# Kernel optimization log

Measured on AMD Instinct MI355X. Metric: run time of the kernel, lower is better.

Reference implementation:

```python
import jax, jax.numpy as jnp
import numpy as np

N, C, H, W = 8, 19, 512, 512
BORDER_DILATE = 5
BORDER_POWER = 0.5
BORDER_WEIGHT = 1.0
IGNORE = 255


def setup_inputs() -> dict:
    key = jax.random.key(0)
    k1, k2 = jax.random.split(key)
    slices = jax.random.normal(k1, (N, C, H, W), dtype=jnp.float32)
    targets = jax.random.randint(k2, (N, 1, H, W), 0, C).astype(jnp.int64)
    return {"slices": slices, "targets": targets}


def class_boundaries(m):
    # m: bool (N, K, H, W); XOR of vertical/horizontal neighbors, padded like torch
    tb = m[:, :, 1:, :] ^ m[:, :, :-1, :]          # pad bottom row with 0
    lr = m[:, :, :, 1:] ^ m[:, :, :, :-1]          # pad leftmost column with 0
    tb = jnp.pad(tb, ((0, 0), (0, 0), (0, 1), (0, 0)))
    lr = jnp.pad(lr, ((0, 0), (0, 0), (0, 0), (1, 0)))
    return tb | lr


def _min_scan_axis(d, axis):
    # forward then backward chamfer pass d[i] = min(d[i], d[i -/+ 1] + 1) along `axis`
    x = jnp.moveaxis(d, axis, 0)

    def step(carry, row):
        new = jnp.minimum(row, carry + 1.0)
        return new, new

    _, fwd = jax.lax.scan(step, x[0], x[1:])
    x = jnp.concatenate([x[:1], fwd], axis=0)
    _, bwd = jax.lax.scan(step, x[-1], x[:-1][::-1])
    x = jnp.concatenate([bwd[::-1], x[-1:]], axis=0)
    return jnp.moveaxis(x, 0, axis)


def distance_matrix(border):
    # border: bool (N, K, H, W). Penalty matches torch.tensor((N,1,H,W)).sum()
    penalty = jnp.float32(N + 1 + H + W)
    d = jnp.where(border, 0.0, penalty)
    d = _min_scan_axis(d, 2)   # H forward + backward
    d = _min_scan_axis(d, 3)   # W forward + backward
    return jax.nn.relu(d - jnp.float32(BORDER_DILATE))


def _forward(slices, targets):
    t = targets[:, 0]  # (N, H, W)
    # cross-entropy, reduction='sum', ignore_index
    logp = jax.nn.log_softmax(slices, axis=1)
    valid = t != IGNORE
    t_safe = jnp.where(valid, t, 0)
    picked = jnp.take_along_axis(logp, t_safe[:, None], axis=1)[:, 0]  # (N,H,W)
    ce = -jnp.sum(jnp.where(valid, picked, 0.0))

    # border loss: vectorized over all class ids (torch loops over unique targets)
    sm = jax.nn.softmax(slices, axis=1)                      # (N,C,H,W)
    pred = jnp.argmax(slices, axis=1, keepdims=True)         # (N,1,H,W)
    cls = jnp.arange(C)[None, :, None, None]
    pred_oh = pred == cls                                    # (N,C,H,W) bool
    tgt_oh = targets == cls                                  # (N,C,H,W) bool
    pred_b = class_boundaries(pred_oh).astype(sm.dtype)
    tgt_d = distance_matrix(class_boundaries(tgt_oh))
    present = jnp.any(tgt_oh, axis=(0, 2, 3)).astype(sm.dtype)  # only ids in targets
    border = jnp.sum(sm * pred_b * tgt_d * present[None, :, None, None])

    return ce + jnp.float32(BORDER_WEIGHT) * border ** jnp.float32(BORDER_POWER)


def reference(slices, targets):
    return _forward(slices, targets)
```

## Files before the change

### kernel.cpp

```cpp
#include <hip/hip_runtime.h>

#define NN 8
#define CC 19
#define HH 512
#define WW 512
#define HW (HH*WW)
#define NPIX (NN*HW)
#define NPLANE (NN*CC)
#define BIGV (1<<20)
#define M7 0x7F7F7F7Fu

__device__ unsigned char g_tT[NPIX];
__device__ unsigned char g_pred[NPIX];
__device__ float g_lse[NPIX];
__device__ unsigned char g_inter[(size_t)NPLANE*HW];
__device__ unsigned char g_pbb[(size_t)NPLANE*HW/8];
__device__ float g_ce;
__device__ float g_part[64][16];
__device__ unsigned int g_present_mask;

__device__ __forceinline__ unsigned int eqz(unsigned int x) {
  unsigned int y = (x & M7) + M7;
  return ~(y | x | M7);
}

__global__ __launch_bounds__(256) void k_pixel(const float* __restrict__ slices,
                                               const int* __restrict__ targets) {
  int bp = blockIdx.x * 2048;
  int n = bp >> 18;
  int r = bp & (HW - 1);
  int wv = threadIdx.x >> 6;
  int lane = threadIdx.x & 63;
  int o0 = wv * 512 + lane * 4;
  int o1 = o0 + 256;
  const float* base = slices + (size_t)n * CC * HW + r;

  const int4* t4p = (const int4*)(targets + bp);
  int4 ta = t4p[o0 >> 2];
  int4 tb = t4p[o1 >> 2];
  int t[8] = {ta.x, ta.y, ta.z, ta.w, tb.x, tb.y, tb.z, tb.w};

  float m[8], s[8], pk[8];
  int a[8];
  {
    float4 x0 = *(const float4*)(base + o0);
    float4 x1 = *(const float4*)(base + o1);
    float x[8] = {x0.x, x0.y, x0.z, x0.w, x1.x, x1.y, x1.z, x1.w};
#pragma unroll
    for (int j = 0; j < 8; ++j) {
      m[j] = x[j];
      a[j] = 0;
      s[j] = __expf(x[j]);
      pk[j] = (t[j] == 0) ? x[j] : 0.f;
    }
  }
#pragma unroll 2
  for (int c = 1; c < CC; ++c) {
    float4 x0 = *(const float4*)(base + (size_t)c * HW + o0);
    float4 x1 = *(const float4*)(base + (size_t)c * HW + o1);
    float x[8] = {x0.x, x0.y, x0.z, x0.w, x1.x, x1.y, x1.z, x1.w};
#pragma unroll
    for (int j = 0; j < 8; ++j) {
      if (x[j] > m[j]) { m[j] = x[j]; a[j] = c; }
      s[j] += __expf(x[j]);
      pk[j] = (c == t[j]) ? x[j] : pk[j];
    }
  }

  float l[8];
  float ce_local = 0.f;
  unsigned int msk = 0u;
#pragma unroll
  for (int j = 0; j < 8; ++j) {
    l[j] = __logf(s[j]);
    if (t[j] != 255) ce_local += l[j] - pk[j];
    if ((unsigned)t[j] < CC) msk |= 1u << t[j];
  }

  ((float4*)(g_lse + bp))[o0 >> 2] = make_float4(l[0], l[1], l[2], l[3]);
  ((float4*)(g_lse + bp))[o1 >> 2] = make_float4(l[4], l[5], l[6], l[7]);
  ((uchar4*)(g_pred + bp))[o0 >> 2] =
      make_uchar4((unsigned char)a[0], (unsigned char)a[1],
                  (unsigned char)a[2], (unsigned char)a[3]);
  ((uchar4*)(g_pred + bp))[o1 >> 2] =
      make_uchar4((unsigned char)a[4], (unsigned char)a[5],
                  (unsigned char)a[6], (unsigned char)a[7]);
#pragma unroll
  for (int j = 0; j < 8; ++j) {
    int p = bp + ((j < 4) ? (o0 + j) : (o1 + j - 4));
    int h = (p >> 9) & 511;
    int w = p & 511;
    g_tT[((size_t)n << 18) + (size_t)w * HH + h] = (unsigned char)t[j];
  }

  __shared__ float sred[256];
  __shared__ unsigned int smsk[256];
  sred[threadIdx.x] = ce_local;
  smsk[threadIdx.x] = msk;
  __syncthreads();
  for (int st = 128; st > 0; st >>= 1) {
    if (threadIdx.x < st) {
      sred[threadIdx.x] += sred[threadIdx.x + st];
      smsk[threadIdx.x] |= smsk[threadIdx.x + st];
    }
    __syncthreads();
  }
  if (threadIdx.x == 0) {
    atomicAdd(&g_ce, sred[0]);
    atomicOr(&g_present_mask, smsk[0]);
  }
}

__global__ __launch_bounds__(512) void k_pbb() {
  int plane = blockIdx.x >> 3;
  int wt = blockIdx.x & 7;
  int c = plane % CC;
  int n = plane / CC;
  int h = threadIdx.x;

  const unsigned char* row = g_pred + ((size_t)n * HH + h) * WW + wt * 64;
  const unsigned char* rown = (h + 1 < HH) ? row + WW : row;

  uint4 c0 = *(const uint4*)(row);
  uint4 c1 = *(const uint4*)(row + 16);
  uint4 c2 = *(const uint4*)(row + 32);
  uint4 c3 = *(const uint4*)(row + 48);
  uint4 n0 = *(const uint4*)(rown);
  uint4 n1 = *(const uint4*)(rown + 16);
  uint4 n2 = *(const uint4*)(rown + 32);
  uint4 n3 = *(const uint4*)(rown + 48);
  unsigned int cwv[16] = {c0.x,c0.y,c0.z,c0.w, c1.x,c1.y,c1.z,c1.w,
                          c2.x,c2.y,c2.z,c2.w, c3.x,c3.y,c3.z,c3.w};
  unsigned int nwv[16] = {n0.x,n0.y,n0.z,n0.w, n1.x,n1.y,n1.z,n1.w,
                          n2.x,n2.y,n2.z,n2.w, n3.x,n3.y,n3.z,n3.w};
  int leftb = (wt > 0) ? (int)row[-1] : (int)(cwv[0] & 255u);

  unsigned char outb[8];
  int pl = leftb;
#pragma unroll
  for (int j = 0; j < 8; ++j) {
    unsigned int bits = 0u;
#pragma unroll
    for (int k = 0; k < 8; ++k) {
      int q = j * 8 + k;
      int pc = (int)((cwv[q >> 2] >> ((q & 3) * 8)) & 255u);
      int pn = (int)((nwv[q >> 2] >> ((q & 3) * 8)) & 255u);
      bool ec = (pc == c);
      bool bb = (ec != (pn == c)) || (ec != (pl == c));
      bits |= (bb ? 1u : 0u) << k;
      pl = pc;
    }
    outb[j] = (unsigned char)bits;
  }
  unsigned char* dst = g_pbb + (((size_t)plane * 8 + wt) * HH + h) * 8;
  *(uint2*)dst = *(const uint2*)outb;
}

__global__ __launch_bounds__(512, 4) void k_hscan() {
  int plane = blockIdx.x >> 3;
  int wt = blockIdx.x & 7;
  int hc = threadIdx.x >> 6;
  int wl = threadIdx.x & 63;
  int c = plane % CC;
  int n = plane / CC;
  int w = wt * 64 + wl;
  const unsigned char* colC = g_tT + ((size_t)n << 18) + (size_t)w * HH + hc * 64;

  uint4 ca = *(const uint4*)(colC);
  uint4 cb = *(const uint4*)(colC + 16);
  uint4 cc2 = *(const uint4*)(colC + 32);
  uint4 cd = *(const uint4*)(colC + 48);
  unsigned int cw[16];
  cw[0]=ca.x; cw[1]=ca.y; cw[2]=ca.z; cw[3]=ca.w;
  cw[4]=cb.x; cw[5]=cb.y; cw[6]=cb.z; cw[7]=cb.w;
  cw[8]=cc2.x; cw[9]=cc2.y; cw[10]=cc2.z; cw[11]=cc2.w;
  cw[12]=cd.x; cw[13]=cd.y; cw[14]=cd.z; cw[15]=cd.w;

  unsigned int lw[16];
#pragma unroll
  for (int i = 0; i < 16; ++i) lw[i] = __shfl_up(cw[i], 1, 64);
  if (wl == 0) {
    if (w > 0) {
      const unsigned char* colL = colC - HH;
      uint4 la = *(const uint4*)(colL);
      uint4 lb = *(const uint4*)(colL + 16);
      uint4 lc = *(const uint4*)(colL + 32);
      uint4 ld = *(const uint4*)(colL + 48);
      lw[0]=la.x; lw[1]=la.y; lw[2]=la.z; lw[3]=la.w;
      lw[4]=lb.x; lw[5]=lb.y; lw[6]=lb.z; lw[7]=lb.w;
      lw[8]=lc.x; lw[9]=lc.y; lw[10]=lc.z; lw[11]=lc.w;
      lw[12]=ld.x; lw[13]=ld.y; lw[14]=ld.z; lw[15]=ld.w;
    } else {
#pragma unroll
      for (int i = 0; i < 16; ++i) lw[i] = cw[i];
    }
  }

  __shared__ unsigned char s_edge[8][64];
  s_edge[hc][wl] = (unsigned char)(cw[0] & 255u);
  __syncthreads();
  unsigned int tnl = (hc < 7) ? (unsigned int)s_edge[hc + 1][wl]
                              : ((cw[15] >> 24) & 255u);

  unsigned int bc = (unsigned int)c * 0x01010101u;
  int v[64];
  int prev = BIGV;
#pragma unroll
  for (int i = 0; i < 16; ++i) {
    unsigned int cwi = cw[i];
    unsigned int nxt = (i < 15) ? (cw[i + 1] & 255u) : tnl;
    unsigned int tnw = (cwi >> 8) | (nxt << 24);
    unsigned int zc = eqz(cwi ^ bc);
    unsigned int zn = eqz(tnw ^ bc);
    unsigned int zl = eqz(lw[i] ^ bc);
    unsigned int bb = (zc ^ zn) | (zc ^ zl);
#pragma unroll
    for (int k = 0; k < 4; ++k) {
      int bit = (int)((bb >> (8 * k + 7)) & 1u);
      prev = min(bit ? 0 : 255, prev + 1);
      v[4 * i + k] = prev;
    }
  }

  __shared__ int s_car[8][64];
  s_car[hc][wl] = v[63];
  __syncthreads();
  int F = BIGV;
#pragma unroll
  for (int i = 0; i < 7; ++i)
    if (i < hc) F = min(s_car[i][wl] + 1, F + 64);
#pragma unroll
  for (int k = 0; k < 64; ++k) v[k] = min(v[k], F + k);

#pragma unroll
  for (int k = 62; k >= 0; --k) v[k] = min(v[k], v[k + 1] + 1);

  __syncthreads();
  s_car[hc][wl] = v[0];
  __syncthreads();
  int B = BIGV;
#pragma unroll
  for (int j = 7; j >= 1; --j)
    if (j > hc) B = min(s_car[j][wl] + 1, B + 64);

  unsigned char* outb = g_inter + (((size_t)plane * 8 + wt) * HH + hc * 64) * 64 + wl;
#pragma unroll
  for (int k = 0; k < 64; ++k) {
    int outv = min(v[k], B + (63 - k));
    outb[(size_t)k * 64] = (unsigned char)outv;
  }
}

__global__ __launch_bounds__(512) void k_wscan(const float* __restrict__ slices) {
  int plane = blockIdx.x >> 6;
  int hg = blockIdx.x & 63;
  int wv = threadIdx.x >> 6;
  int lane = threadIdx.x & 63;
  int h = hg * 8 + wv;
  int c = plane % CC;
  int n = plane / CC;

  const unsigned char* rowp =
      g_inter + (((size_t)plane * 8 + (lane >> 3)) * HH + h) * 64 + (lane & 7) * 8;
  uint2 r8 = *(const uint2*)rowp;
  unsigned int pbb = (unsigned int)
      g_pbb[(((size_t)plane * 8 + (lane >> 3)) * HH + h) * 8 + (lane & 7)];

  int d0[8];
#pragma unroll
  for (int k = 0; k < 4; ++k) {
    d0[k]     = (int)((r8.x >> (k * 8)) & 255u);
    d0[k + 4] = (int)((r8.y >> (k * 8)) & 255u);
  }
  int ls[8];
  ls[0] = d0[0];
#pragma unroll
  for (int k = 1; k < 8; ++k) ls[k] = min(d0[k], ls[k - 1] + 1);
  int u = ls[7] - 8 * lane;
#pragma unroll
  for (int o = 1; o < 64; o <<= 1) {
    int t = __shfl_up(u, o, 64);
    if (lane >= o) u = min(u, t);
  }
  int cf = __shfl_up(u, 1, 64);
  int carry = (lane == 0) ? BIGV : cf + 8 * (lane - 1);
  int f[8];
#pragma unroll
  for (int k = 0; k < 8; ++k) f[k] = min(ls[k], carry + k + 1);
  int bs[8];
  bs[7] = f[7];
#pragma unroll
  for (int k = 6; k >= 0; --k) bs[k] = min(f[k], bs[k + 1] + 1);
  int mm = bs[0] + 8 * lane;
#pragma unroll
  for (int o = 1; o < 64; o <<= 1) {
    int t = __shfl_down(mm, o, 64);
    if (lane + o < 64) mm = min(mm, t);
  }
  int mb = __shfl_down(mm, 1, 64);
  int carryb = (lane == 63) ? BIGV : mb - 8 * lane;

  float acc = 0.f;
#pragma unroll
  for (int k = 0; k < 8; ++k) {
    int D = min(bs[k], carryb - k);
    int d = D - 5;
    if (d > 0 && ((pbb >> k) & 1u)) {
      int w = lane * 8 + k;
      int pix = (n * HH + h) * WW + w;
      float x = slices[((size_t)n * CC + c) * HW + (size_t)h * WW + w];
      float smv = __expf(x - g_lse[pix]);
      acc += smv * (float)d;
    }
  }

#pragma unroll
  for (int o = 32; o > 0; o >>= 1) acc += __shfl_down(acc, o, 64);
  if (lane == 0) {
    float pres = (g_present_mask >> c) & 1u ? 1.f : 0.f;
    atomicAdd(&g_part[blockIdx.x & 63][0], acc * pres);
  }
}

__global__ void k_final(float* __restrict__ out) {
  int t = threadIdx.x;
  float b = g_part[t][0];
#pragma unroll
  for (int o = 32; o > 0; o >>= 1) b += __shfl_down(b, o, 64);
  if (t == 0) {
    out[0] = g_ce + sqrtf(b);
    g_ce = 0.f;
    g_present_mask = 0u;
  }
  g_part[t][0] = 0.f;
}

extern "C" void kernel_launch(void* const* d_in, const int* in_sizes, int n_in,
                              void* d_out, int out_size, void* d_ws, size_t ws_size,
                              hipStream_t stream) {
  const float* slices = (const float*)d_in[0];
  const int* targets = (const int*)d_in[1];
  float* out = (float*)d_out;
  (void)d_ws; (void)ws_size; (void)in_sizes; (void)n_in; (void)out_size;

  hipLaunchKernelGGL(k_pixel, dim3(NPIX / 2048), dim3(256), 0, stream, slices, targets);
  hipLaunchKernelGGL(k_pbb, dim3(NPLANE * 8), dim3(512), 0, stream);
  hipLaunchKernelGGL(k_hscan, dim3(NPLANE * 8), dim3(512), 0, stream);
  hipLaunchKernelGGL(k_wscan, dim3(NPLANE * 64), dim3(512), 0, stream, slices);
  hipLaunchKernelGGL(k_final, dim3(1), dim3(64), 0, stream, out);
}
```

Before: 117.9 us.

## Fuse pred-border kernel into hscan, stage target tile in LDS, fold final reduction

Merges the predicted-boundary bitmask computation into the horizontal scan kernel, which removes one launch. The transposed target tile is now staged through shared memory with a padded stride, so each column and its left neighbour are read from LDS instead of coalescing-poor global loads and shuffles. The final reduction kernel is replaced by a last-block-done pattern using an atomic counter inside k_wscan, which saves another launch. The cost is a large 33KB LDS allocation in k_hscan, which may lower occupancy, plus extra fences and atomics at the end of every wscan block.

Measured after the change: 347.0 us. 194% more time.

```diff
diff --git a/kernel.cpp b/kernel.cpp
--- a/kernel.cpp
+++ b/kernel.cpp
@@ -18,6 +18,7 @@
 __device__ float g_ce;
 __device__ float g_part[64][16];
 __device__ unsigned int g_present_mask;
+__device__ unsigned int g_done;
 
 __device__ __forceinline__ unsigned int eqz(unsigned int x) {
   unsigned int y = (x & M7) + M7;
@@ -111,51 +112,7 @@
   }
 }
 
-__global__ __launch_bounds__(512) void k_pbb() {
-  int plane = blockIdx.x >> 3;
-  int wt = blockIdx.x & 7;
-  int c = plane % CC;
-  int n = plane / CC;
-  int h = threadIdx.x;
-
-  const unsigned char* row = g_pred + ((size_t)n * HH + h) * WW + wt * 64;
-  const unsigned char* rown = (h + 1 < HH) ? row + WW : row;
-
-  uint4 c0 = *(const uint4*)(row);
-  uint4 c1 = *(const uint4*)(row + 16);
-  uint4 c2 = *(const uint4*)(row + 32);
-  uint4 c3 = *(const uint4*)(row + 48);
-  uint4 n0 = *(const uint4*)(rown);
-  uint4 n1 = *(const uint4*)(rown + 16);
-  uint4 n2 = *(const uint4*)(rown + 32);
-  uint4 n3 = *(const uint4*)(rown + 48);
-  unsigned int cwv[16] = {c0.x,c0.y,c0.z,c0.w, c1.x,c1.y,c1.z,c1.w,
-                          c2.x,c2.y,c2.z,c2.w, c3.x,c3.y,c3.z,c3.w};
-  unsigned int nwv[16] = {n0.x,n0.y,n0.z,n0.w, n1.x,n1.y,n1.z,n1.w,
-                          n2.x,n2.y,n2.z,n2.w, n3.x,n3.y,n3.z,n3.w};
-  int leftb = (wt > 0) ? (int)row[-1] : (int)(cwv[0] & 255u);
-
-  unsigned char outb[8];
-  int pl = leftb;
-#pragma unroll
-  for (int j = 0; j < 8; ++j) {
-    unsigned int bits = 0u;
-#pragma unroll
-    for (int k = 0; k < 8; ++k) {
-      int q = j * 8 + k;
-      int pc = (int)((cwv[q >> 2] >> ((q & 3) * 8)) & 255u);
-      int pn = (int)((nwv[q >> 2] >> ((q & 3) * 8)) & 255u);
-      bool ec = (pc == c);
-      bool bb = (ec != (pn == c)) || (ec != (pl == c));
-      bits |= (bb ? 1u : 0u) << k;
-      pl = pc;
-    }
-    outb[j] = (unsigned char)bits;
-  }
-  unsigned char* dst = g_pbb + (((size_t)plane * 8 + wt) * HH + h) * 8;
-  *(uint2*)dst = *(const uint2*)outb;
-}
-
+#define CSTRIDE 528
 __global__ __launch_bounds__(512, 4) void k_hscan() {
   int plane = blockIdx.x >> 3;
   int wt = blockIdx.x & 7;
@@ -164,42 +121,85 @@
   int c = plane % CC;
   int n = plane / CC;
   int w = wt * 64 + wl;
-  const unsigned char* colC = g_tT + ((size_t)n << 18) + (size_t)w * HH + hc * 64;
-
-  uint4 ca = *(const uint4*)(colC);
-  uint4 cb = *(const uint4*)(colC + 16);
-  uint4 cc2 = *(const uint4*)(colC + 32);
-  uint4 cd = *(const uint4*)(colC + 48);
+
+  __shared__ unsigned char s_tile[64 * CSTRIDE];
+
+  {
+    int h2 = threadIdx.x;
+    const unsigned char* row = g_pred + ((size_t)n * HH + h2) * WW + wt * 64;
+    const unsigned char* rown = (h2 + 1 < HH) ? row + WW : row;
+    uint4 c0 = *(const uint4*)(row);
+    uint4 c1 = *(const uint4*)(row + 16);
+    uint4 c2 = *(const uint4*)(row + 32);
+    uint4 c3 = *(const uint4*)(row + 48);
+    uint4 n0 = *(const uint4*)(rown);
+    uint4 n1 = *(const uint4*)(rown + 16);
+    uint4 n2 = *(const uint4*)(rown + 32);
+    uint4 n3 = *(const uint4*)(rown + 48);
+    unsigned int cwv[16] = {c0.x,c0.y,c0.z,c0.w, c1.x,c1.y,c1.z,c1.w,
+                            c2.x,c2.y,c2.z,c2.w, c3.x,c3.y,c3.z,c3.w};
+    unsigned int nwv[16] = {n0.x,n0.y,n0.z,n0.w, n1.x,n1.y,n1.z,n1.w,
+                            n2.x,n2.y,n2.z,n2.w, n3.x,n3.y,n3.z,n3.w};
+    int pl = (wt > 0) ? (int)row[-1] : (int)(cwv[0] & 255u);
+    unsigned int w0 = 0u, w1 = 0u;
+#pragma unroll
+    for (int q = 0; q < 64; ++q) {
+      int pc = (int)((cwv[q >> 2] >> ((q & 3) * 8)) & 255u);
+      int pn = (int)((nwv[q >> 2] >> ((q & 3) * 8)) & 255u);
+      bool ec = (pc == c);
+      bool bb = (ec != (pn == c)) || (ec != (pl == c));
+      if (q < 32) w0 |= (bb ? 1u : 0u) << q;
+      else        w1 |= (bb ? 1u : 0u) << (q - 32);
+      pl = pc;
+    }
+    unsigned char* dst = g_pbb + (((size_t)plane * 8 + wt) * HH + h2) * 8;
+    *(uint2*)dst = make_uint2(w0, w1);
+  }
+
+  {
+    const unsigned char* src =
+        g_tT + ((size_t)n << 18) + (size_t)wt * 32768 + threadIdx.x * 64;
+    int col = threadIdx.x >> 3;
+    int off = (threadIdx.x & 7) * 64;
+    uint4 a = *(const uint4*)(src);
+    uint4 b = *(const uint4*)(src + 16);
+    uint4 c4 = *(const uint4*)(src + 32);
+    uint4 d = *(const uint4*)(src + 48);
+    unsigned char* dst = s_tile + col * CSTRIDE + off;
+    *(uint4*)(dst)      = a;
+    *(uint4*)(dst + 16) = b;
+    *(uint4*)(dst + 32) = c4;
+    *(uint4*)(dst + 48) = d;
+  }
+  __syncthreads();
+
+  const unsigned char* myCol = s_tile + wl * CSTRIDE + hc * 64;
   unsigned int cw[16];
-  cw[0]=ca.x; cw[1]=ca.y; cw[2]=ca.z; cw[3]=ca.w;
-  cw[4]=cb.x; cw[5]=cb.y; cw[6]=cb.z; cw[7]=cb.w;
-  cw[8]=cc2.x; cw[9]=cc2.y; cw[10]=cc2.z; cw[11]=cc2.w;
-  cw[12]=cd.x; cw[13]=cd.y; cw[14]=cd.z; cw[15]=cd.w;
-
+#pragma unroll
+  for (int i = 0; i < 4; ++i) {
+    uint4 q = *(const uint4*)(myCol + i * 16);
+    cw[4*i] = q.x; cw[4*i+1] = q.y; cw[4*i+2] = q.z; cw[4*i+3] = q.w;
+  }
   unsigned int lw[16];
-#pragma unroll
-  for (int i = 0; i < 16; ++i) lw[i] = __shfl_up(cw[i], 1, 64);
-  if (wl == 0) {
-    if (w > 0) {
-      const unsigned char* colL = colC - HH;
-      uint4 la = *(const uint4*)(colL);
-      uint4 lb = *(const uint4*)(colL + 16);
-      uint4 lc = *(const uint4*)(colL + 32);
-      uint4 ld = *(const uint4*)(colL + 48);
-      lw[0]=la.x; lw[1]=la.y; lw[2]=la.z; lw[3]=la.w;
-      lw[4]=lb.x; lw[5]=lb.y; lw[6]=lb.z; lw[7]=lb.w;
-      lw[8]=lc.x; lw[9]=lc.y; lw[10]=lc.z; lw[11]=lc.w;
-      lw[12]=ld.x; lw[13]=ld.y; lw[14]=ld.z; lw[15]=ld.w;
-    } else {
-#pragma unroll
-      for (int i = 0; i < 16; ++i) lw[i] = cw[i];
-    }
-  }
-
-  __shared__ unsigned char s_edge[8][64];
-  s_edge[hc][wl] = (unsigned char)(cw[0] & 255u);
-  __syncthreads();
-  unsigned int tnl = (hc < 7) ? (unsigned int)s_edge[hc + 1][wl]
+  if (wl > 0) {
+    const unsigned char* lcol = s_tile + (wl - 1) * CSTRIDE + hc * 64;
+#pragma unroll
+    for (int i = 0; i < 4; ++i) {
+      uint4 q = *(const uint4*)(lcol + i * 16);
+      lw[4*i] = q.x; lw[4*i+1] = q.y; lw[4*i+2] = q.z; lw[4*i+3] = q.w;
+    }
+  } else if (w > 0) {
+    const unsigned char* colL = g_tT + ((size_t)n << 18) + (size_t)(w - 1) * HH + hc * 64;
+#pragma unroll
+    for (int i = 0; i < 4; ++i) {
+      uint4 q = *(const uint4*)(colL + i * 16);
+      lw[4*i] = q.x; lw[4*i+1] = q.y; lw[4*i+2] = q.z; lw[4*i+3] = q.w;
+    }
+  } else {
+#pragma unroll
+    for (int i = 0; i < 16; ++i) lw[i] = cw[i];
+  }
+  unsigned int tnl = (hc < 7) ? (unsigned int)myCol[64]
                               : ((cw[15] >> 24) & 255u);
 
   unsigned int bc = (unsigned int)c * 0x01010101u;
@@ -251,7 +251,8 @@
   }
 }
 
-__global__ __launch_bounds__(512) void k_wscan(const float* __restrict__ slices) {
+__global__ __launch_bounds__(512) void k_wscan(const float* __restrict__ slices,
+                                               float* __restrict__ out) {
   int plane = blockIdx.x >> 6;
   int hg = blockIdx.x & 63;
   int wv = threadIdx.x >> 6;
@@ -320,19 +321,28 @@
     float pres = (g_present_mask >> c) & 1u ? 1.f : 0.f;
     atomicAdd(&g_part[blockIdx.x & 63][0], acc * pres);
   }
-}
-
-__global__ void k_final(float* __restrict__ out) {
-  int t = threadIdx.x;
-  float b = g_part[t][0];
-#pragma unroll
-  for (int o = 32; o > 0; o >>= 1) b += __shfl_down(b, o, 64);
-  if (t == 0) {
-    out[0] = g_ce + sqrtf(b);
-    g_ce = 0.f;
-    g_present_mask = 0u;
-  }
-  g_part[t][0] = 0.f;
+
+  __shared__ int s_last;
+  __syncthreads();
+  if (threadIdx.x == 0) {
+    __threadfence();
+    unsigned int old = atomicAdd(&g_done, 1u);
+    s_last = (old == (unsigned int)(gridDim.x - 1)) ? 1 : 0;
+  }
+  __syncthreads();
+  if (s_last && threadIdx.x < 64) {
+    __threadfence();
+    float b = atomicAdd(&g_part[threadIdx.x][0], 0.f);
+#pragma unroll
+    for (int o = 32; o > 0; o >>= 1) b += __shfl_down(b, o, 64);
+    if (threadIdx.x == 0) {
+      out[0] = g_ce + sqrtf(b);
+      g_ce = 0.f;
+      g_present_mask = 0u;
+      g_done = 0u;
+    }
+    g_part[threadIdx.x][0] = 0.f;
+  }
 }
 
 extern "C" void kernel_launch(void* const* d_in, const int* in_sizes, int n_in,
@@ -344,8 +354,6 @@
   (void)d_ws; (void)ws_size; (void)in_sizes; (void)n_in; (void)out_size;
 
   hipLaunchKernelGGL(k_pixel, dim3(NPIX / 2048), dim3(256), 0, stream, slices, targets);
-  hipLaunchKernelGGL(k_pbb, dim3(NPLANE * 8), dim3(512), 0, stream);
   hipLaunchKernelGGL(k_hscan, dim3(NPLANE * 8), dim3(512), 0, stream);
-  hipLaunchKernelGGL(k_wscan, dim3(NPLANE * 64), dim3(512), 0, stream, slices);
-  hipLaunchKernelGGL(k_final, dim3(1), dim3(64), 0, stream, out);
-}
+  hipLaunchKernelGGL(k_wscan, dim3(NPLANE * 64), dim3(512), 0, stream, slices, out);
+}
```
